# Kernel tuning notes

Hardware: AMD Instinct MI355X
Metric: run time of the kernel (lower is better)

## Reference

```python
import jax, jax.numpy as jnp
import numpy as np

B, H, S, D = 2, 16, 2048, 64

def setup_inputs() -> dict:
    key = jax.random.key(0)
    kq, kk, kv = jax.random.split(key, 3)
    Q = jax.random.normal(kq, (B, H, S, D), dtype=jnp.float32)
    K = jax.random.normal(kk, (B, H, S, D), dtype=jnp.float32)
    V = jax.random.normal(kv, (B, H, S, D), dtype=jnp.float32)
    # causal mask, broadcastable over batch/head dims (True = keep)
    mask = jnp.tril(jnp.ones((S, S), dtype=jnp.bool_))
    return {"Q": Q, "K": K, "V": V, "mask": mask}

def reference(Q, K, V, mask):
    scale = jax.lax.rsqrt(jnp.float32(Q.shape[-1]))
    # [b, h, q, k] attention logits
    at = jnp.einsum('bhqd,bhkd->bhqk', Q, K) * scale
    at = jnp.where(mask, at, -jnp.inf)
    # manual numerically-stable softmax (matches SoftMax module)
    x_max = jnp.max(at, axis=-1, keepdims=True)
    x_exp = jnp.exp(at - x_max)
    scores = x_exp / jnp.sum(x_exp, axis=-1, keepdims=True)
    return jnp.einsum('bhqk,bhkd->bhqd', scores, V)
```

## Files before the change

### kernel.cpp

```cpp
#include <hip/hip_runtime.h>
#include <math.h>

typedef __attribute__((ext_vector_type(8))) short bf16x8;
typedef __attribute__((ext_vector_type(8))) short s16x8;
typedef __attribute__((ext_vector_type(4))) short s16x4;
typedef __attribute__((ext_vector_type(4))) float f32x4;
typedef __attribute__((ext_vector_type(16))) float f32x16;

namespace {
constexpr int kS   = 2048;
constexpr int kD   = 64;
constexpr int kBH  = 32;
constexpr int kT   = kS / 64;
constexpr int PPAD = 72;
constexpr float kScaleLog2e = 0.125f * 1.44269504088896340736f;
}

__device__ __forceinline__ short f2bf(float f) {
    union { float f; unsigned u; } c; c.f = f;
    unsigned r = c.u + 0x7fffu + ((c.u >> 16) & 1u);
    return (short)(r >> 16);
}

__device__ __forceinline__ s16x8 pack8(const float4& a, const float4& b) {
    s16x8 r;
    r[0] = f2bf(a.x); r[1] = f2bf(a.y); r[2] = f2bf(a.z); r[3] = f2bf(a.w);
    r[4] = f2bf(b.x); r[5] = f2bf(b.y); r[6] = f2bf(b.z); r[7] = f2bf(b.w);
    return r;
}

__device__ __forceinline__ unsigned cvtpk(float lo, float hi_) {
    unsigned r;
    asm("v_cvt_pk_bf16_f32 %0, %1, %2" : "=v"(r) : "v"(lo), "v"(hi_));
    return r;
}
__device__ __forceinline__ void plswap(unsigned& a, unsigned& b) {
    asm("v_permlane32_swap_b32 %0, %1" : "+v"(a), "+v"(b));
}

__global__ __launch_bounds__(256)
void prepack(const float* __restrict__ K, const float* __restrict__ V,
             short* __restrict__ wsK, short* __restrict__ wsVT)
{
    __shared__ float vt[64][65];
    const int tid = threadIdx.x;
    const int kb  = blockIdx.x;
    const int bh  = blockIdx.y;
    const int r   = tid >> 2;
    const int s   = tid & 3;
    const int c0  = s * 16;

    const size_t grow = ((size_t)bh * kS + (size_t)kb * 64 + r) * kD + c0;
    const size_t tbase = ((size_t)bh * kT + kb) * 4096;

    {
        const float4* kr = (const float4*)(K + grow);
        float4 a = kr[0], b = kr[1], c = kr[2], d = kr[3];
        const int kt = r >> 5, ql = r & 31;
        short* out = wsK + tbase + (size_t)((s * 2 + kt) * 64) * 8;
        *(s16x8*)(out + (size_t)ql * 8)        = pack8(a, b);
        *(s16x8*)(out + (size_t)(32 + ql) * 8) = pack8(c, d);
    }
    {
        const float4* vr = (const float4*)(V + grow);
        float4 a = vr[0], b = vr[1], c = vr[2], d = vr[3];
        float t[16] = {a.x,a.y,a.z,a.w, b.x,b.y,b.z,b.w,
                       c.x,c.y,c.z,c.w, d.x,d.y,d.z,d.w};
        #pragma unroll
        for (int jj = 0; jj < 16; ++jj) vt[r][c0 + jj] = t[jj];
    }
    __syncthreads();
    {
        const int d     = tid >> 2;
        const int slice = tid & 3;
        const int k0    = slice * 16;
        const int dt = d >> 5, ql = d & 31;
        s16x8 g0, g1;
        #pragma unroll
        for (int jj = 0; jj < 8; ++jj) g0[jj] = f2bf(vt[k0 + jj][d]);
        #pragma unroll
        for (int jj = 0; jj < 8; ++jj) g1[jj] = f2bf(vt[k0 + 8 + jj][d]);
        short* out = wsVT + tbase + (size_t)((slice * 2 + dt) * 64) * 8;
        *(s16x8*)(out + (size_t)ql * 8)        = g0;
        *(s16x8*)(out + (size_t)(32 + ql) * 8) = g1;
    }
}

__global__ __launch_bounds__(128)
void attn_v9(const float* __restrict__ Q, const short* __restrict__ wsK,
             const short* __restrict__ wsVT, float* __restrict__ O)
{
    __shared__ float4 mO[8][64];
    __shared__ float  mL[64];

    const int tid  = threadIdx.x;
    const int w    = tid >> 6;
    const int lane = tid & 63;
    const int ql   = lane & 31;
    const int hi   = lane >> 5;

    const int n   = (int)blockIdx.x;
    const int xcd = n & 7;
    const int j   = n >> 3;
    const int bh  = xcd * 4 + (j >> 5);
    const int p   = j & 31;

    const int T1 = ((63 - p) >> 1) + 1;
    const int T2 = (p >> 1) + 1;

    const char* Kroot = (const char*)wsK + (size_t)bh * kT * 8192;
    const char* Vroot = (const char*)wsVT + (size_t)bh * kT * 8192;

    f32x16 zero16;
    #pragma unroll
    for (int c = 0; c < 16; ++c) zero16[c] = 0.f;

    f32x16 o[2];
    float  l_;

    auto loadK = [&](int kb, bf16x8 (&kf)[8]) {
        const char* kp = Kroot + (size_t)kb * 8192 + lane * 16;
        #pragma unroll
        for (int i = 0; i < 8; ++i)
            kf[i] = *(const bf16x8*)(kp + i * 1024);
    };

    auto process = [&](int qs, int kb0, int kb1) {
        if (kb0 >= kb1) return;
        const int Tdiag = (qs >> 1) + 1;
        const int qrow  = qs * 32 + ql;

        const float* Qr = Q + ((size_t)bh * kS + qrow) * kD;
        bf16x8 qf[4];
        #pragma unroll
        for (int s = 0; s < 4; ++s) {
            const float4 a = *(const float4*)(Qr + s * 16 + hi * 8);
            const float4 b = *(const float4*)(Qr + s * 16 + hi * 8 + 4);
            bf16x8 f;
            f[0] = f2bf(a.x * kScaleLog2e); f[1] = f2bf(a.y * kScaleLog2e);
            f[2] = f2bf(a.z * kScaleLog2e); f[3] = f2bf(a.w * kScaleLog2e);
            f[4] = f2bf(b.x * kScaleLog2e); f[5] = f2bf(b.y * kScaleLog2e);
            f[6] = f2bf(b.z * kScaleLog2e); f[7] = f2bf(b.w * kScaleLog2e);
            qf[s] = f;
        }

        bf16x8 kA[8], kB[8];
        loadK(kb0, kA);

        auto tile = [&](bf16x8 (&kcur)[8], bf16x8 (&knxt)[8], int kb) {
            bf16x8 vf[8];
            {
                const char* vp = Vroot + (size_t)kb * 8192 + lane * 16;
                #pragma unroll
                for (int i = 0; i < 8; ++i)
                    vf[i] = *(const bf16x8*)(vp + i * 1024);
            }

            f32x16 sacc[2] = {zero16, zero16};
            #pragma unroll
            for (int kt = 0; kt < 2; ++kt)
                #pragma unroll
                for (int s = 0; s < 4; ++s)
                    sacc[kt] = __builtin_amdgcn_mfma_f32_32x32x16_bf16(
                        kcur[s * 2 + kt], qf[s], sacc[kt], 0, 0, 0);

            if (kb + 1 < kb1) loadK(kb + 1, knxt);

            if (kb == Tdiag - 1) {
                #pragma unroll
                for (int kt = 0; kt < 2; ++kt) {
                    const int kbase = kb * 64 + kt * 32 + 4 * hi;
                    #pragma unroll
                    for (int c = 0; c < 16; ++c) {
                        const int kg = kbase + (c & 3) + 8 * (c >> 2);
                        if (kg > qrow) sacc[kt][c] = -1e30f;
                    }
                }
            }

            float psum = 0.f;
            #pragma unroll
            for (int kt = 0; kt < 2; ++kt)
                #pragma unroll
                for (int c = 0; c < 16; ++c) {
                    const float pe = exp2f(sacc[kt][c]);
                    sacc[kt][c] = pe;
                    psum += pe;
                }
            l_ += psum;

            #pragma unroll
            for (int kt = 0; kt < 2; ++kt) {
                unsigned w8[8];
                #pragma unroll
                for (int i = 0; i < 8; ++i)
                    w8[i] = cvtpk(sacc[kt][2 * i], sacc[kt][2 * i + 1]);
                #pragma unroll
                for (int s = 0; s < 2; ++s) {
                    unsigned A0 = w8[4 * s + 0], B0 = w8[4 * s + 2];
                    unsigned A1 = w8[4 * s + 1], B1 = w8[4 * s + 3];
                    plswap(A0, B0);
                    plswap(A1, B1);
                    union { unsigned u[4]; bf16x8 v; } pk;
                    pk.u[0] = A0; pk.u[1] = A1; pk.u[2] = B0; pk.u[3] = B1;
                    #pragma unroll
                    for (int dt = 0; dt < 2; ++dt)
                        o[dt] = __builtin_amdgcn_mfma_f32_32x32x16_bf16(
                            vf[(kt * 2 + s) * 2 + dt], pk.v, o[dt], 0, 0, 0);
                }
            }
        };

        int kb = kb0;
        #pragma unroll 1
        while (true) {
            tile(kA, kB, kb);
            if (++kb == kb1) break;
            tile(kB, kA, kb);
            if (++kb == kb1) break;
        }
    };

    auto store_strip = [&](int qs) {
        const float l   = l_ + __shfl_xor(l_, 32);
        const float inv = 1.0f / l;
        float* Ob = O + ((size_t)bh * kS + qs * 32 + ql) * kD;
        #pragma unroll
        for (int dt = 0; dt < 2; ++dt)
            #pragma unroll
            for (int t = 0; t < 4; ++t) {
                float4 v;
                v.x = o[dt][4 * t + 0] * inv;
                v.y = o[dt][4 * t + 1] * inv;
                v.z = o[dt][4 * t + 2] * inv;
                v.w = o[dt][4 * t + 3] * inv;
                *(float4*)(Ob + dt * 32 + 4 * hi + 8 * t) = v;
            }
    };

    if (w == 0) {
        o[0] = zero16; o[1] = zero16; l_ = 0.f;
        process(63 - p, 0, 17);
    } else {
        o[0] = zero16; o[1] = zero16; l_ = 0.f;
        process(p, 0, T2);
        store_strip(p);
        o[0] = zero16; o[1] = zero16; l_ = 0.f;
        process(63 - p, 17, T1);
        #pragma unroll
        for (int dt = 0; dt < 2; ++dt)
            #pragma unroll
            for (int t = 0; t < 4; ++t) {
                float4 v;
                v.x = o[dt][4 * t + 0];
                v.y = o[dt][4 * t + 1];
                v.z = o[dt][4 * t + 2];
                v.w = o[dt][4 * t + 3];
                mO[dt * 4 + t][lane] = v;
            }
        mL[lane] = l_;
    }

    __syncthreads();

    if (w == 0) {
        #pragma unroll
        for (int dt = 0; dt < 2; ++dt)
            #pragma unroll
            for (int t = 0; t < 4; ++t) {
                const float4 v = mO[dt * 4 + t][lane];
                o[dt][4 * t + 0] += v.x;
                o[dt][4 * t + 1] += v.y;
                o[dt][4 * t + 2] += v.z;
                o[dt][4 * t + 3] += v.w;
            }
        l_ += mL[lane];
        store_strip(63 - p);
    }
}

__global__ __launch_bounds__(256)
void attn_mfma(const float* __restrict__ Q, const float* __restrict__ K,
               const float* __restrict__ V, float* __restrict__ O)
{
    __shared__ short Klds[64 * PPAD];
    __shared__ short VTlds[64 * PPAD];
    __shared__ short Plds[4 * 16 * PPAD];

    const int tid  = threadIdx.x;
    const int lane = tid & 63;
    const int w    = tid >> 6;
    const int lo   = lane & 15;
    const int hi   = lane >> 4;
    const int qt = (int)gridDim.x - 1 - (int)blockIdx.x;
    const int bh = blockIdx.y;
    const size_t hbase = (size_t)bh * kS * kD;

    const float* Qr = Q + hbase + (size_t)(qt * 64 + w * 16 + lo) * kD;
    bf16x8 qfrag[2];
    #pragma unroll
    for (int dc = 0; dc < 2; ++dc) {
        const float4 a = *(const float4*)(Qr + dc * 32 + hi * 8);
        const float4 b = *(const float4*)(Qr + dc * 32 + hi * 8 + 4);
        bf16x8 f;
        f[0] = f2bf(a.x * kScaleLog2e); f[1] = f2bf(a.y * kScaleLog2e);
        f[2] = f2bf(a.z * kScaleLog2e); f[3] = f2bf(a.w * kScaleLog2e);
        f[4] = f2bf(b.x * kScaleLog2e); f[5] = f2bf(b.y * kScaleLog2e);
        f[6] = f2bf(b.z * kScaleLog2e); f[7] = f2bf(b.w * kScaleLog2e);
        qfrag[dc] = f;
    }

    const f32x4 zero4 = {0.f, 0.f, 0.f, 0.f};
    f32x4 o[4] = {zero4, zero4, zero4, zero4};
    float m_[4] = {-1e30f, -1e30f, -1e30f, -1e30f};
    float l_[4] = {0.f, 0.f, 0.f, 0.f};
    const int sr = tid >> 2;
    const int sc = (tid & 3) * 16;
    const float* Kg = K + hbase;
    const float* Vg = V + hbase;
    short* Pw = &Plds[w * 16 * PPAD];

    for (int kb = 0; kb <= qt; ++kb) {
        __syncthreads();
        {
            const float* krow = Kg + (size_t)(kb * 64 + sr) * kD + sc;
            const float* vrow = Vg + (size_t)(kb * 64 + sr) * kD + sc;
            #pragma unroll
            for (int i = 0; i < 4; ++i) {
                const float4 kv = ((const float4*)krow)[i];
                s16x4 ks;
                ks[0] = f2bf(kv.x); ks[1] = f2bf(kv.y);
                ks[2] = f2bf(kv.z); ks[3] = f2bf(kv.w);
                *(s16x4*)&Klds[sr * PPAD + sc + i * 4] = ks;
                const float4 vv = ((const float4*)vrow)[i];
                VTlds[(sc + i * 4 + 0) * PPAD + sr] = f2bf(vv.x);
                VTlds[(sc + i * 4 + 1) * PPAD + sr] = f2bf(vv.y);
                VTlds[(sc + i * 4 + 2) * PPAD + sr] = f2bf(vv.z);
                VTlds[(sc + i * 4 + 3) * PPAD + sr] = f2bf(vv.w);
            }
        }
        __syncthreads();

        f32x4 sacc[4] = {zero4, zero4, zero4, zero4};
        #pragma unroll
        for (int kk = 0; kk < 4; ++kk)
            #pragma unroll
            for (int dc = 0; dc < 2; ++dc) {
                const bf16x8 kf = *(const bf16x8*)(
                    &Klds[(kk * 16 + lo) * PPAD + dc * 32 + hi * 8]);
                sacc[kk] = __builtin_amdgcn_mfma_f32_16x16x32_bf16(
                    qfrag[dc], kf, sacc[kk], 0, 0, 0);
            }
        if (kb == qt) {
            #pragma unroll
            for (int kk = 0; kk < 4; ++kk)
                #pragma unroll
                for (int r = 0; r < 4; ++r)
                    if (kk * 16 + lo > w * 16 + hi * 4 + r) sacc[kk][r] = -1e30f;
        }
        float nm[4], alpha[4];
        #pragma unroll
        for (int r = 0; r < 4; ++r) {
            float v = fmaxf(fmaxf(sacc[0][r], sacc[1][r]),
                            fmaxf(sacc[2][r], sacc[3][r]));
            v = fmaxf(v, __shfl_xor(v, 1));
            v = fmaxf(v, __shfl_xor(v, 2));
            v = fmaxf(v, __shfl_xor(v, 4));
            v = fmaxf(v, __shfl_xor(v, 8));
            nm[r]    = fmaxf(v, m_[r]);
            alpha[r] = exp2f(m_[r] - nm[r]);
        }
        float p[4][4];
        #pragma unroll
        for (int kk = 0; kk < 4; ++kk)
            #pragma unroll
            for (int r = 0; r < 4; ++r)
                p[kk][r] = exp2f(sacc[kk][r] - nm[r]);
        #pragma unroll
        for (int r = 0; r < 4; ++r) {
            float s = (p[0][r] + p[1][r]) + (p[2][r] + p[3][r]);
            s += __shfl_xor(s, 1);
            s += __shfl_xor(s, 2);
            s += __shfl_xor(s, 4);
            s += __shfl_xor(s, 8);
            l_[r] = l_[r] * alpha[r] + s;
            m_[r] = nm[r];
        }
        #pragma unroll
        for (int dcB = 0; dcB < 4; ++dcB)
            #pragma unroll
            for (int r = 0; r < 4; ++r)
                o[dcB][r] *= alpha[r];
        #pragma unroll
        for (int kk = 0; kk < 4; ++kk)
            #pragma unroll
            for (int r = 0; r < 4; ++r)
                Pw[(hi * 4 + r) * PPAD + kk * 16 + lo] = f2bf(p[kk][r]);
        #pragma unroll
        for (int kc = 0; kc < 2; ++kc) {
            const bf16x8 pf = *(const bf16x8*)(&Pw[lo * PPAD + kc * 32 + hi * 8]);
            #pragma unroll
            for (int dcB = 0; dcB < 4; ++dcB) {
                const bf16x8 vf = *(const bf16x8*)(
                    &VTlds[(dcB * 16 + lo) * PPAD + kc * 32 + hi * 8]);
                o[dcB] = __builtin_amdgcn_mfma_f32_16x16x32_bf16(
                    pf, vf, o[dcB], 0, 0, 0);
            }
        }
    }
    float* Ob = O + hbase;
    #pragma unroll
    for (int r = 0; r < 4; ++r) {
        const float inv = 1.0f / l_[r];
        const size_t q = (size_t)(qt * 64 + w * 16 + hi * 4 + r);
        #pragma unroll
        for (int dcB = 0; dcB < 4; ++dcB)
            Ob[q * kD + dcB * 16 + lo] = o[dcB][r] * inv;
    }
}

extern "C" void kernel_launch(void* const* d_in, const int* in_sizes, int n_in,
                              void* d_out, int out_size, void* d_ws, size_t ws_size,
                              hipStream_t stream) {
    const float* Q = (const float*)d_in[0];
    const float* K = (const float*)d_in[1];
    const float* V = (const float*)d_in[2];
    float* out = (float*)d_out;
    (void)in_sizes; (void)n_in; (void)out_size;

    const size_t elemsK   = (size_t)kBH * kS * kD;
    const size_t need_pre = elemsK * 2 * sizeof(short);

    if (ws_size >= need_pre) {
        short* wsK  = (short*)d_ws;
        short* wsVT = wsK + elemsK;
        prepack<<<dim3(kT, kBH), 256, 0, stream>>>(K, V, wsK, wsVT);
        attn_v9<<<dim3(1024), 128, 0, stream>>>(Q, wsK, wsVT, out);
    } else {
        attn_mfma<<<dim3(kT, kBH), 256, 0, stream>>>(Q, K, V, out);
    }
}
```

Measured before the change: 51.68 us.

## Process paired 32-row query strips per wave to reuse K/V fragments

Each wave now handles two adjacent 32-row query strips (64 rows) against each K/V tile, so every loaded K and V fragment feeds twice as many MFMAs. The grid is halved to 512 blocks, and the long/short strip balancing is rebuilt around pairs. The K double buffer is replaced by a single in-place prefetch buffer, and the exp sums use split accumulators. In exchange, register pressure rises (launch bounds set to one block per SIMD), there are fewer blocks to spread across CUs, and prefetch overlap may be reduced.

Result: slower. 53.60 us (+3.7%).

```diff
diff --git a/kernel.cpp b/kernel.cpp
--- a/kernel.cpp
+++ b/kernel.cpp
@@ -86,12 +86,12 @@
     }
 }
 
-__global__ __launch_bounds__(128)
-void attn_v9(const float* __restrict__ Q, const short* __restrict__ wsK,
-             const short* __restrict__ wsVT, float* __restrict__ O)
+__global__ __launch_bounds__(128, 1)
+void attn_v10(const float* __restrict__ Q, const short* __restrict__ wsK,
+              const short* __restrict__ wsVT, float* __restrict__ O)
 {
-    __shared__ float4 mO[8][64];
-    __shared__ float  mL[64];
+    __shared__ float4 mO[16][64];
+    __shared__ float  mL[2][64];
 
     const int tid  = threadIdx.x;
     const int w    = tid >> 6;
@@ -102,11 +102,8 @@
     const int n   = (int)blockIdx.x;
     const int xcd = n & 7;
     const int j   = n >> 3;
-    const int bh  = xcd * 4 + (j >> 5);
-    const int p   = j & 31;
-
-    const int T1 = ((63 - p) >> 1) + 1;
-    const int T2 = (p >> 1) + 1;
+    const int bh  = xcd * 4 + (j & 3);
+    const int u   = j >> 2;
 
     const char* Kroot = (const char*)wsK + (size_t)bh * kT * 8192;
     const char* Vroot = (const char*)wsVT + (size_t)bh * kT * 8192;
@@ -115,23 +112,11 @@
     #pragma unroll
     for (int c = 0; c < 16; ++c) zero16[c] = 0.f;
 
-    f32x16 o[2];
-    float  l_;
-
-    auto loadK = [&](int kb, bf16x8 (&kf)[8]) {
-        const char* kp = Kroot + (size_t)kb * 8192 + lane * 16;
-        #pragma unroll
-        for (int i = 0; i < 8; ++i)
-            kf[i] = *(const bf16x8*)(kp + i * 1024);
-    };
-
-    auto process = [&](int qs, int kb0, int kb1) {
-        if (kb0 >= kb1) return;
-        const int Tdiag = (qs >> 1) + 1;
-        const int qrow  = qs * 32 + ql;
-
+    f32x16 oA[2], oB[2];
+    float  lA, lB;
+
+    auto loadQ = [&](int qrow, bf16x8 (&qf)[4]) {
         const float* Qr = Q + ((size_t)bh * kS + qrow) * kD;
-        bf16x8 qf[4];
         #pragma unroll
         for (int s = 0; s < 4; ++s) {
             const float4 a = *(const float4*)(Qr + s * 16 + hi * 8);
@@ -143,11 +128,30 @@
             f[6] = f2bf(b.z * kScaleLog2e); f[7] = f2bf(b.w * kScaleLog2e);
             qf[s] = f;
         }
-
-        bf16x8 kA[8], kB[8];
-        loadK(kb0, kA);
-
-        auto tile = [&](bf16x8 (&kcur)[8], bf16x8 (&knxt)[8], int kb) {
+    };
+
+    auto loadK = [&](int kb, bf16x8 (&kf)[8]) {
+        const char* kp = Kroot + (size_t)kb * 8192 + lane * 16;
+        #pragma unroll
+        for (int i = 0; i < 8; ++i)
+            kf[i] = *(const bf16x8*)(kp + i * 1024);
+    };
+
+    auto processPair = [&](int s0, int kb0, int kb1) {
+        if (kb0 >= kb1) return;
+        const int Td    = (s0 >> 1) + 1;
+        const int qrowA = s0 * 32 + ql;
+        const int qrowB = qrowA + 32;
+
+        bf16x8 qa[4], qb[4];
+        loadQ(qrowA, qa);
+        loadQ(qrowB, qb);
+
+        bf16x8 kc[8];
+        loadK(kb0, kc);
+
+        #pragma unroll 1
+        for (int kb = kb0; kb < kb1; ++kb) {
             bf16x8 vf[8];
             {
                 const char* vp = Vroot + (size_t)kb * 8192 + lane * 16;
@@ -156,72 +160,92 @@
                     vf[i] = *(const bf16x8*)(vp + i * 1024);
             }
 
-            f32x16 sacc[2] = {zero16, zero16};
+            f32x16 sA[2] = {zero16, zero16};
+            f32x16 sB[2] = {zero16, zero16};
             #pragma unroll
             for (int kt = 0; kt < 2; ++kt)
                 #pragma unroll
-                for (int s = 0; s < 4; ++s)
-                    sacc[kt] = __builtin_amdgcn_mfma_f32_32x32x16_bf16(
-                        kcur[s * 2 + kt], qf[s], sacc[kt], 0, 0, 0);
-
-            if (kb + 1 < kb1) loadK(kb + 1, knxt);
-
-            if (kb == Tdiag - 1) {
+                for (int s = 0; s < 4; ++s) {
+                    sA[kt] = __builtin_amdgcn_mfma_f32_32x32x16_bf16(
+                        kc[s * 2 + kt], qa[s], sA[kt], 0, 0, 0);
+                    sB[kt] = __builtin_amdgcn_mfma_f32_32x32x16_bf16(
+                        kc[s * 2 + kt], qb[s], sB[kt], 0, 0, 0);
+                }
+
+            if (kb + 1 < kb1) loadK(kb + 1, kc);
+
+            if (kb == Td - 1) {
                 #pragma unroll
                 for (int kt = 0; kt < 2; ++kt) {
                     const int kbase = kb * 64 + kt * 32 + 4 * hi;
                     #pragma unroll
                     for (int c = 0; c < 16; ++c) {
                         const int kg = kbase + (c & 3) + 8 * (c >> 2);
-                        if (kg > qrow) sacc[kt][c] = -1e30f;
+                        if (kg > qrowA) sA[kt][c] = -1e30f;
+                        if (kg > qrowB) sB[kt][c] = -1e30f;
                     }
                 }
             }
 
-            float psum = 0.f;
+            float a0 = 0.f, a1 = 0.f, a2 = 0.f, a3 = 0.f;
+            float b0 = 0.f, b1 = 0.f, b2 = 0.f, b3 = 0.f;
             #pragma unroll
             for (int kt = 0; kt < 2; ++kt)
                 #pragma unroll
-                for (int c = 0; c < 16; ++c) {
-                    const float pe = exp2f(sacc[kt][c]);
-                    sacc[kt][c] = pe;
-                    psum += pe;
+                for (int c = 0; c < 16; c += 4) {
+                    float pa0 = exp2f(sA[kt][c + 0]);
+                    float pa1 = exp2f(sA[kt][c + 1]);
+                    float pa2 = exp2f(sA[kt][c + 2]);
+                    float pa3 = exp2f(sA[kt][c + 3]);
+                    sA[kt][c + 0] = pa0; sA[kt][c + 1] = pa1;
+                    sA[kt][c + 2] = pa2; sA[kt][c + 3] = pa3;
+                    a0 += pa0; a1 += pa1; a2 += pa2; a3 += pa3;
+                    float pb0 = exp2f(sB[kt][c + 0]);
+                    float pb1 = exp2f(sB[kt][c + 1]);
+                    float pb2 = exp2f(sB[kt][c + 2]);
+                    float pb3 = exp2f(sB[kt][c + 3]);
+                    sB[kt][c + 0] = pb0; sB[kt][c + 1] = pb1;
+                    sB[kt][c + 2] = pb2; sB[kt][c + 3] = pb3;
+                    b0 += pb0; b1 += pb1; b2 += pb2; b3 += pb3;
                 }
-            l_ += psum;
+            lA += (a0 + a1) + (a2 + a3);
+            lB += (b0 + b1) + (b2 + b3);
 
             #pragma unroll
             for (int kt = 0; kt < 2; ++kt) {
-                unsigned w8[8];
-                #pragma unroll
-                for (int i = 0; i < 8; ++i)
-                    w8[i] = cvtpk(sacc[kt][2 * i], sacc[kt][2 * i + 1]);
+                unsigned wa[8], wb[8];
+                #pragma unroll
+                for (int i = 0; i < 8; ++i) {
+                    wa[i] = cvtpk(sA[kt][2 * i], sA[kt][2 * i + 1]);
+                    wb[i] = cvtpk(sB[kt][2 * i], sB[kt][2 * i + 1]);
+                }
                 #pragma unroll
                 for (int s = 0; s < 2; ++s) {
-                    unsigned A0 = w8[4 * s + 0], B0 = w8[4 * s + 2];
-                    unsigned A1 = w8[4 * s + 1], B1 = w8[4 * s + 3];
-                    plswap(A0, B0);
-                    plswap(A1, B1);
-                    union { unsigned u[4]; bf16x8 v; } pk;
-                    pk.u[0] = A0; pk.u[1] = A1; pk.u[2] = B0; pk.u[3] = B1;
+                    unsigned A0 = wa[4 * s + 0], A2 = wa[4 * s + 2];
+                    unsigned A1 = wa[4 * s + 1], A3 = wa[4 * s + 3];
+                    plswap(A0, A2);
+                    plswap(A1, A3);
+                    union { unsigned u4[4]; bf16x8 v; } pa;
+                    pa.u4[0] = A0; pa.u4[1] = A1; pa.u4[2] = A2; pa.u4[3] = A3;
+                    unsigned B0 = wb[4 * s + 0], B2 = wb[4 * s + 2];
+                    unsigned B1 = wb[4 * s + 1], B3 = wb[4 * s + 3];
+                    plswap(B0, B2);
+                    plswap(B1, B3);
+                    union { unsigned u4[4]; bf16x8 v; } pb;
+                    pb.u4[0] = B0; pb.u4[1] = B1; pb.u4[2] = B2; pb.u4[3] = B3;
                     #pragma unroll
-                    for (int dt = 0; dt < 2; ++dt)
-                        o[dt] = __builtin_amdgcn_mfma_f32_32x32x16_bf16(
-                            vf[(kt * 2 + s) * 2 + dt], pk.v, o[dt], 0, 0, 0);
+                    for (int dt = 0; dt < 2; ++dt) {
+                        oA[dt] = __builtin_amdgcn_mfma_f32_32x32x16_bf16(
+                            vf[(kt * 2 + s) * 2 + dt], pa.v, oA[dt], 0, 0, 0);
+                        oB[dt] = __builtin_amdgcn_mfma_f32_32x32x16_bf16(
+                            vf[(kt * 2 + s) * 2 + dt], pb.v, oB[dt], 0, 0, 0);
+                    }
                 }
             }
-        };
-
-        int kb = kb0;
-        #pragma unroll 1
-        while (true) {
-            tile(kA, kB, kb);
-            if (++kb == kb1) break;
-            tile(kB, kA, kb);
-            if (++kb == kb1) break;
         }
     };
 
-    auto store_strip = [&](int qs) {
+    auto storeStrip = [&](int qs, f32x16 (&o)[2], float l_) {
         const float l   = l_ + __shfl_xor(l_, 32);
         const float inv = 1.0f / l;
         float* Ob = O + ((size_t)bh * kS + qs * 32 + ql) * kD;
@@ -238,27 +262,36 @@
             }
     };
 
+    const int sLong = 62 - 2 * u;
+    const int sShort = 2 * u;
+
     if (w == 0) {
-        o[0] = zero16; o[1] = zero16; l_ = 0.f;
-        process(63 - p, 0, 17);
+        oA[0] = zero16; oA[1] = zero16; oB[0] = zero16; oB[1] = zero16;
+        lA = 0.f; lB = 0.f;
+        processPair(sLong, 0, 17);
     } else {
-        o[0] = zero16; o[1] = zero16; l_ = 0.f;
-        process(p, 0, T2);
-        store_strip(p);
-        o[0] = zero16; o[1] = zero16; l_ = 0.f;
-        process(63 - p, 17, T1);
+        oA[0] = zero16; oA[1] = zero16; oB[0] = zero16; oB[1] = zero16;
+        lA = 0.f; lB = 0.f;
+        processPair(sShort, 0, u + 1);
+        storeStrip(sShort,     oA, lA);
+        storeStrip(sShort + 1, oB, lB);
+        oA[0] = zero16; oA[1] = zero16; oB[0] = zero16; oB[1] = zero16;
+        lA = 0.f; lB = 0.f;
+        processPair(sLong, 17, 32 - u);
         #pragma unroll
         for (int dt = 0; dt < 2; ++dt)
             #pragma unroll
             for (int t = 0; t < 4; ++t) {
-                float4 v;
-                v.x = o[dt][4 * t + 0];
-                v.y = o[dt][4 * t + 1];
-                v.z = o[dt][4 * t + 2];
-                v.w = o[dt][4 * t + 3];
-                mO[dt * 4 + t][lane] = v;
-            }
-        mL[lane] = l_;
+                float4 va, vb;
+                va.x = oA[dt][4 * t + 0]; va.y = oA[dt][4 * t + 1];
+                va.z = oA[dt][4 * t + 2]; va.w = oA[dt][4 * t + 3];
+                vb.x = oB[dt][4 * t + 0]; vb.y = oB[dt][4 * t + 1];
+                vb.z = oB[dt][4 * t + 2]; vb.w = oB[dt][4 * t + 3];
+                mO[dt * 4 + t][lane]     = va;
+                mO[8 + dt * 4 + t][lane] = vb;
+            }
+        mL[0][lane] = lA;
+        mL[1][lane] = lB;
     }
 
     __syncthreads();
@@ -268,14 +301,17 @@
         for (int dt = 0; dt < 2; ++dt)
             #pragma unroll
             for (int t = 0; t < 4; ++t) {
-                const float4 v = mO[dt * 4 + t][lane];
-                o[dt][4 * t + 0] += v.x;
-                o[dt][4 * t + 1] += v.y;
-                o[dt][4 * t + 2] += v.z;
-                o[dt][4 * t + 3] += v.w;
-            }
-        l_ += mL[lane];
-        store_strip(63 - p);
+                const float4 va = mO[dt * 4 + t][lane];
+                const float4 vb = mO[8 + dt * 4 + t][lane];
+                oA[dt][4 * t + 0] += va.x; oA[dt][4 * t + 1] += va.y;
+                oA[dt][4 * t + 2] += va.z; oA[dt][4 * t + 3] += va.w;
+                oB[dt][4 * t + 0] += vb.x; oB[dt][4 * t + 1] += vb.y;
+                oB[dt][4 * t + 2] += vb.z; oB[dt][4 * t + 3] += vb.w;
+            }
+        lA += mL[0][lane];
+        lB += mL[1][lane];
+        storeStrip(sLong,     oA, lA);
+        storeStrip(sLong + 1, oB, lB);
     }
 }
 
@@ -435,7 +471,7 @@
         short* wsK  = (short*)d_ws;
         short* wsVT = wsK + elemsK;
         prepack<<<dim3(kT, kBH), 256, 0, stream>>>(K, V, wsK, wsVT);
-        attn_v9<<<dim3(1024), 128, 0, stream>>>(Q, wsK, wsVT, out);
+        attn_v10<<<dim3(512), 128, 0, stream>>>(Q, wsK, wsVT, out);
     } else {
         attn_mfma<<<dim3(kT, kBH), 256, 0, stream>>>(Q, K, V, out);
     }
```
